# Optimization experiments

Measured on AMD Instinct MI355X. Metric: run time of the kernel, lower is better.

## Reference

```python
import jax, jax.numpy as jnp
import numpy as np

B = 16384
C = 1000  # num_classes
H = 128   # adapter hidden


def setup_inputs() -> dict:
    key = jax.random.key(0)
    k1, k2, k3 = jax.random.split(key, 3)
    logits = jax.random.normal(k1, (B, C), dtype=jnp.float32)
    # adapter_net params: Linear(C->H) -> ReLU -> Linear(H->C); stored as x @ W + b
    W1 = jax.random.normal(k2, (C, H), dtype=jnp.float32) * 0.03
    b1 = jnp.zeros((H,), dtype=jnp.float32)
    W2 = jax.random.normal(k3, (H, C), dtype=jnp.float32) * 0.03
    b2 = jnp.zeros((C,), dtype=jnp.float32)
    return {"logits": logits, "W1": W1, "b1": b1, "W2": W2, "b2": b2}


def reference(logits, W1, b1, W2, b2):
    prob = jax.nn.softmax(logits, axis=-1)                       # [B, C]
    # descending sort
    order = jnp.argsort(-prob, axis=-1)                          # [B, C] int
    sorted_prob = jnp.take_along_axis(prob, order, axis=-1)      # [B, C]
    # diffs between consecutive sorted probs, last column = 1
    diffs = jnp.concatenate(
        [sorted_prob[:, :-1] - sorted_prob[:, 1:],
         jnp.ones((prob.shape[0], 1), dtype=prob.dtype)], axis=-1)
    # adapter net on prob
    h = jax.nn.relu(prob @ W1 + b1)                              # [B, H]
    cal = h @ W2 + b2                                            # [B, C]
    cal = jnp.concatenate([jax.nn.sigmoid(cal[:, :-1]), cal[:, -1:]], axis=-1)
    c = diffs * cal                                              # [B, C]
    # U @ c  (U upper-triangular ones) == reverse cumulative sum along last dim
    rev_cumsum = jnp.cumsum(c[:, ::-1], axis=-1)[:, ::-1]        # [B, C]
    # S.T @ v scatters sorted-position values back to original class positions
    inv_order = jnp.argsort(order, axis=-1)                      # inverse permutation
    fitted = jnp.take_along_axis(rev_cumsum, inv_order, axis=-1)
    return fitted + logits
```

## Files before the change

kernel.cpp:

```cpp
#include <hip/hip_runtime.h>
#include <hip/hip_bf16.h>
#include <math.h>

#define B_ROWS 16384
#define C_CLS  1000
#define H_DIM  128
#define NEG_BIG (-3.0e38f)

#define MT    16
#define PSTR  1064
#define CSTR  1064
#define HSTR  136
#define KT1   32
#define CT1   8
#define KT2   4
#define CT2   64

#define QSCALE 511.0f
#define QINV   (1.0f / 511.0f)

typedef __attribute__((ext_vector_type(8))) short short8;
typedef __attribute__((ext_vector_type(4))) float f32x4;

__device__ __forceinline__ unsigned short f2bf(float x) {
    unsigned int u = __float_as_uint(x);
    unsigned int r = (u + 0x7FFFu + ((u >> 16) & 1u)) >> 16;
    return (unsigned short)r;
}
__device__ __forceinline__ float bf2f(unsigned short v) {
    return __uint_as_float(((unsigned int)v) << 16);
}
__device__ __forceinline__ float sigm(float x) {
    return 1.0f / (1.0f + __expf(-x));
}
__device__ __forceinline__ unsigned int umin(unsigned int a, unsigned int b) {
    return a < b ? a : b;
}
__device__ __forceinline__ int SKU(int i) { return i + (i >> 4); }
__device__ __forceinline__ int PSL(unsigned int b) {
    return (int)((b >> 3) + (b & 7u) * 64u);
}

__global__ __launch_bounds__(256) void pack_kernel(
    const float* __restrict__ W1, const float* __restrict__ W2,
    unsigned short* __restrict__ W1p, unsigned short* __restrict__ W2p)
{
    const int t = blockIdx.x * 256 + threadIdx.x;
    if (t < 16384) {
        const int lane = t & 63, slot = t >> 6;
        const int kt = slot >> 3, ct = slot & 7;
        const int col = ct * 16 + (lane & 15);
        const int k0 = kt * 32 + (lane >> 4) * 8;
        unsigned short v[8];
        #pragma unroll
        for (int j = 0; j < 8; ++j) {
            int k = k0 + j;
            v[j] = f2bf((k < C_CLS) ? W1[k * H_DIM + col] : 0.f);
        }
        #pragma unroll
        for (int j = 0; j < 8; ++j) W1p[(size_t)t * 8 + j] = v[j];
    } else {
        const int t2 = t - 16384;
        const int lane = t2 & 63, slot = t2 >> 6;
        const int kt = slot >> 6, ct = slot & 63;
        const int col = ct * 16 + (lane & 15);
        const int k0 = kt * 32 + (lane >> 4) * 8;
        unsigned short v[8];
        #pragma unroll
        for (int j = 0; j < 8; ++j) {
            int k = k0 + j;
            v[j] = f2bf((col < C_CLS) ? W2[k * C_CLS + col] : 0.f);
        }
        #pragma unroll
        for (int j = 0; j < 8; ++j) W2p[(size_t)t2 * 8 + j] = v[j];
    }
}

__global__ __launch_bounds__(512) void fused_kernel(
    const float* __restrict__ logits, const float* __restrict__ bias1,
    const float* __restrict__ bias2, const unsigned short* __restrict__ W1p,
    const unsigned short* __restrict__ W2p, float* __restrict__ out)
{
    __shared__ alignas(16) unsigned short probS[MT * PSTR];
    __shared__ alignas(16) unsigned int uniReg[8 * 512];
    __shared__ float qsA[MT], svsA[MT], rowInv[MT], rowLast[MT];

    unsigned short* calS = probS;
    unsigned short* hS = (unsigned short*)uniReg;

    const int tid = threadIdx.x;
    const int w = tid >> 6, lane = tid & 63;
    const size_t row0 = (size_t)blockIdx.x * MT;

    #pragma unroll
    for (int rr = 0; rr < 2; ++rr) {
        const int r = 2 * w + rr;
        const float* lr = logits + (row0 + r) * C_CLS;
        float sum = 0.f, mx = NEG_BIG;
        for (int c4 = lane; c4 < 250; c4 += 64) {
            const float4 x = reinterpret_cast<const float4*>(lr)[c4];
            float e0 = __expf(x.x), e1 = __expf(x.y);
            float e2 = __expf(x.z), e3 = __expf(x.w);
            sum += (e0 + e1) + (e2 + e3);
            mx = fmaxf(mx, fmaxf(fmaxf(x.x, x.y), fmaxf(x.z, x.w)));
            uint2 pk;
            asm("v_cvt_pk_bf16_f32 %0, %1, %2" : "=v"(pk.x) : "v"(e0), "v"(e1));
            asm("v_cvt_pk_bf16_f32 %0, %1, %2" : "=v"(pk.y) : "v"(e2), "v"(e3));
            *reinterpret_cast<uint2*>(&probS[r * PSTR + 4 * c4]) = pk;
        }
        #pragma unroll
        for (int off = 32; off; off >>= 1) {
            sum += __shfl_xor(sum, off);
            mx = fmaxf(mx, __shfl_xor(mx, off));
        }
        if (lane == 0) {
            const float maxe = __expf(mx);
            rowInv[r] = 1.0f / sum;
            qsA[r]  = QSCALE / maxe;
            svsA[r] = maxe * QINV * (1.0f / sum);
        }
        if (lane < 12) *reinterpret_cast<unsigned int*>(&probS[r * PSTR + 1000 + 2 * lane]) = 0u;
    }
    __syncthreads();

    {
        f32x4 acc = {0.f, 0.f, 0.f, 0.f};
        const unsigned short* aptr = probS + (lane & 15) * PSTR + (lane >> 4) * 8;
        #pragma unroll 4
        for (int kt = 0; kt < KT1; ++kt) {
            short8 a = *reinterpret_cast<const short8*>(aptr + kt * 32);
            short8 b = *reinterpret_cast<const short8*>(W1p + ((size_t)(kt * CT1 + w) * 64 + lane) * 8);
            acc = __builtin_amdgcn_mfma_f32_16x16x32_bf16(a, b, acc, 0, 0, 0);
        }
        const int hc = w * 16 + (lane & 15);
        const float bb = bias1[hc];
        #pragma unroll
        for (int i = 0; i < 4; ++i) {
            const int hrow = (lane >> 4) * 4 + i;
            hS[hrow * HSTR + hc] = f2bf(fmaxf(acc[i] * rowInv[hrow] + bb, 0.f));
        }
    }

    unsigned int dP[2][8];
    #pragma unroll
    for (int rr = 0; rr < 2; ++rr) {
        const int r = 2 * w + rr;
        const float qs = qsA[r];
        #pragma unroll
        for (int k = 0; k < 8; ++k) {
            const unsigned int pk =
                *reinterpret_cast<const unsigned int*>(&probS[r * PSTR + 2 * lane + 128 * k]);
            unsigned int d0 = umin((unsigned int)(bf2f((unsigned short)(pk & 0xFFFFu)) * qs), 511u);
            unsigned int d1 = umin((unsigned int)(bf2f((unsigned short)(pk >> 16)) * qs), 511u);
            dP[rr][k] = d0 | (d1 << 16);
        }
    }
    __syncthreads();

    {
        f32x4 acc[8];
        #pragma unroll
        for (int t = 0; t < 8; ++t) acc[t] = (f32x4){0.f, 0.f, 0.f, 0.f};
        const unsigned short* haptr = hS + (lane & 15) * HSTR + (lane >> 4) * 8;
        #pragma unroll
        for (int kt = 0; kt < KT2; ++kt) {
            short8 a = *reinterpret_cast<const short8*>(haptr + kt * 32);
            #pragma unroll
            for (int t = 0; t < 8; ++t) {
                short8 b = *reinterpret_cast<const short8*>(
                    W2p + ((size_t)(kt * CT2 + 8 * w + t) * 64 + lane) * 8);
                acc[t] = __builtin_amdgcn_mfma_f32_16x16x32_bf16(a, b, acc[t], 0, 0, 0);
            }
        }
        #pragma unroll
        for (int t = 0; t < 8; ++t) {
            const int col = (8 * w + t) * 16 + (lane & 15);
            if (col < C_CLS) {
                const int sc = SKU(col);
                #pragma unroll
                for (int i = 0; i < 4; ++i) {
                    const int rloc = (lane >> 4) * 4 + i;
                    float v = acc[t][i] + bias2[col];
                    calS[rloc * CSTR + sc] = f2bf(v);
                    if (col == C_CLS - 1) rowLast[rloc] = v;
                }
            }
        }
    }
    __syncthreads();

    unsigned int* hist = uniReg + w * 512;
    float* Pb = (float*)(uniReg + w * 512);
    const bool act7 = lane < 52;

    #pragma unroll
    for (int rr = 0; rr < 2; ++rr) {
        const int r = 2 * w + rr;
        const float svs = svsA[r];
        const size_t rowbase = (row0 + r) * C_CLS;

        #pragma unroll
        for (int k = 0; k < 4; ++k) hist[64 * k + lane] = 0u;

        #pragma unroll
        for (int k = 0; k < 8; ++k) {
            if (k < 7 || act7) {
                const unsigned int d0 = dP[rr][k] & 0xFFFFu;
                const unsigned int d1 = dP[rr][k] >> 16;
                atomicAdd(&hist[d0 >> 1], 1u << ((d0 & 1u) * 16u));
                atomicAdd(&hist[d1 >> 1], 1u << ((d1 & 1u) * 16u));
            }
        }

        unsigned int c[8], T;
        unsigned int base0;
        {
            uint4 v = *reinterpret_cast<uint4*>(&hist[4 * lane]);
            c[0] = v.x & 0xFFFFu; c[1] = v.x >> 16;
            c[2] = v.y & 0xFFFFu; c[3] = v.y >> 16;
            c[4] = v.z & 0xFFFFu; c[5] = v.z >> 16;
            c[6] = v.w & 0xFFFFu; c[7] = v.w >> 16;
            T = ((c[0] + c[1]) + (c[2] + c[3])) + ((c[4] + c[5]) + (c[6] + c[7]));
            unsigned int x = T;
            #pragma unroll
            for (int off = 1; off < 64; off <<= 1) {
                unsigned int y = __shfl_up(x, off);
                if (lane >= off) x += y;
            }
            base0 = x - T;
        }

        int prev;
        {
            int hiOcc = -1;
            #pragma unroll
            for (int j = 0; j < 8; ++j) if (c[j] > 0) hiOcc = 8 * lane + j;
            int x = hiOcc;
            #pragma unroll
            for (int off = 1; off < 64; off <<= 1) {
                int y = __shfl_up(x, off);
                if (lane >= off) x = max(x, y);
            }
            prev = __shfl_up(x, 1);
            if (lane == 0) prev = -1;
        }

        float s[8];
        float run = 0.f;
        {
            unsigned int brun = base0;
            #pragma unroll
            for (int j = 0; j < 8; ++j) {
                const int b = 8 * lane + j;
                float e = 0.f;
                if (c[j] > 0) {
                    if (brun == 0) {
                        e = rowLast[r];
                    } else {
                        const float cl = bf2f(calS[r * CSTR + SKU((C_CLS - 1) - (int)brun)]);
                        e = (float)(b - prev) * svs * sigm(cl);
                    }
                    prev = b;
                }
                brun += c[j];
                run += e;
                s[j] = run;
            }
        }
        float x = run;
        #pragma unroll
        for (int off = 1; off < 64; off <<= 1) {
            float y = __shfl_up(x, off);
            if (lane >= off) x += y;
        }
        const float X = x - run;

        #pragma unroll
        for (int j = 0; j < 8; ++j) Pb[lane + 64 * j] = X + s[j];

        #pragma unroll
        for (int k = 0; k < 8; ++k) {
            if (k < 7 || act7) {
                const int idx = 2 * lane + 128 * k;
                const float2 xf = *reinterpret_cast<const float2*>(&logits[rowbase + idx]);
                float2 ov;
                ov.x = Pb[PSL(dP[rr][k] & 0xFFFFu)] + xf.x;
                ov.y = Pb[PSL(dP[rr][k] >> 16)] + xf.y;
                *reinterpret_cast<float2*>(&out[rowbase + idx]) = ov;
            }
        }
    }
}

extern "C" void kernel_launch(void* const* d_in, const int* in_sizes, int n_in,
                              void* d_out, int out_size, void* d_ws, size_t ws_size,
                              hipStream_t stream)
{
    const float* logits = (const float*)d_in[0];
    const float* W1     = (const float*)d_in[1];
    const float* b1     = (const float*)d_in[2];
    const float* W2     = (const float*)d_in[3];
    const float* b2     = (const float*)d_in[4];
    float* out = (float*)d_out;

    unsigned short* W1p = (unsigned short*)d_ws;
    unsigned short* W2p = W1p + (size_t)KT1 * CT1 * 64 * 8;

    pack_kernel<<<dim3(128), dim3(256), 0, stream>>>(W1, W2, W1p, W2p);

    fused_kernel<<<dim3(B_ROWS / MT), dim3(512), 0, stream>>>(
        logits, b1, b2, W1p, W2p, out);
}
```

Baseline: 68.14 us.

## Interleave two rows per wave in rank/scatter phase and prefetch logits early

Each wave now processes its two rows at the same time through histogram, scans and scatter, keeping separate shared-memory histogram buffers per row. This gives the scan shuffles more independent work to overlap. The second-pass logits loads are issued at the start of the phase so their global latency hides behind the histogram work. The Pb stride is padded from 64 to 68 to cut LDS bank conflicts. The cost is more registers (32 float2 prefetches plus doubled state) and more shared memory, which may lower occupancy.

```diff
diff --git a/kernel.cpp b/kernel.cpp
--- a/kernel.cpp
+++ b/kernel.cpp
@@ -15,6 +15,7 @@
 #define CT1   8
 #define KT2   4
 #define CT2   64
+#define SLICE 576
 
 #define QSCALE 511.0f
 #define QINV   (1.0f / 511.0f)
@@ -38,7 +39,7 @@
 }
 __device__ __forceinline__ int SKU(int i) { return i + (i >> 4); }
 __device__ __forceinline__ int PSL(unsigned int b) {
-    return (int)((b >> 3) + (b & 7u) * 64u);
+    return (int)((b >> 3) + (b & 7u) * 68u);
 }
 
 __global__ __launch_bounds__(256) void pack_kernel(
@@ -82,7 +83,7 @@
     const unsigned short* __restrict__ W2p, float* __restrict__ out)
 {
     __shared__ alignas(16) unsigned short probS[MT * PSTR];
-    __shared__ alignas(16) unsigned int uniReg[8 * 512];
+    __shared__ alignas(16) unsigned int uniReg[8 * 2 * SLICE];
     __shared__ float qsA[MT], svsA[MT], rowInv[MT], rowLast[MT];
 
     unsigned short* calS = probS;
@@ -189,105 +190,137 @@
     }
     __syncthreads();
 
-    unsigned int* hist = uniReg + w * 512;
-    float* Pb = (float*)(uniReg + w * 512);
+    unsigned int* hist0 = uniReg + (size_t)w * 2 * SLICE;
+    unsigned int* hist1 = hist0 + SLICE;
+    float* Pb0 = (float*)hist0;
+    float* Pb1 = (float*)hist1;
     const bool act7 = lane < 52;
-
+    const size_t rowbase0 = (row0 + 2 * w) * C_CLS;
+    const size_t rowbase1 = rowbase0 + C_CLS;
+
+    float2 xf[2][8];
+    #pragma unroll
+    for (int k = 0; k < 8; ++k) {
+        if (k < 7 || act7) {
+            xf[0][k] = *reinterpret_cast<const float2*>(&logits[rowbase0 + 2 * lane + 128 * k]);
+            xf[1][k] = *reinterpret_cast<const float2*>(&logits[rowbase1 + 2 * lane + 128 * k]);
+        }
+    }
+
+    #pragma unroll
+    for (int k = 0; k < 4; ++k) {
+        hist0[64 * k + lane] = 0u;
+        hist1[64 * k + lane] = 0u;
+    }
+
+    #pragma unroll
+    for (int k = 0; k < 8; ++k) {
+        if (k < 7 || act7) {
+            const unsigned int a0 = dP[0][k] & 0xFFFFu, a1 = dP[0][k] >> 16;
+            atomicAdd(&hist0[a0 >> 1], 1u << ((a0 & 1u) * 16u));
+            atomicAdd(&hist0[a1 >> 1], 1u << ((a1 & 1u) * 16u));
+            const unsigned int b0 = dP[1][k] & 0xFFFFu, b1 = dP[1][k] >> 16;
+            atomicAdd(&hist1[b0 >> 1], 1u << ((b0 & 1u) * 16u));
+            atomicAdd(&hist1[b1 >> 1], 1u << ((b1 & 1u) * 16u));
+        }
+    }
+
+    unsigned int c[2][8], T[2];
+    #pragma unroll
+    for (int rr = 0; rr < 2; ++rr) {
+        uint4 v = *reinterpret_cast<uint4*>(&(rr ? hist1 : hist0)[4 * lane]);
+        c[rr][0] = v.x & 0xFFFFu; c[rr][1] = v.x >> 16;
+        c[rr][2] = v.y & 0xFFFFu; c[rr][3] = v.y >> 16;
+        c[rr][4] = v.z & 0xFFFFu; c[rr][5] = v.z >> 16;
+        c[rr][6] = v.w & 0xFFFFu; c[rr][7] = v.w >> 16;
+        T[rr] = ((c[rr][0] + c[rr][1]) + (c[rr][2] + c[rr][3]))
+              + ((c[rr][4] + c[rr][5]) + (c[rr][6] + c[rr][7]));
+    }
+
+    unsigned int base0_[2];
+    int prev_[2];
+    {
+        unsigned int x0 = T[0], x1 = T[1];
+        int h0 = -1, h1 = -1;
+        #pragma unroll
+        for (int j = 0; j < 8; ++j) {
+            if (c[0][j] > 0) h0 = 8 * lane + j;
+            if (c[1][j] > 0) h1 = 8 * lane + j;
+        }
+        int m0 = h0, m1 = h1;
+        #pragma unroll
+        for (int off = 1; off < 64; off <<= 1) {
+            unsigned int y0 = __shfl_up(x0, off);
+            unsigned int y1 = __shfl_up(x1, off);
+            int n0 = __shfl_up(m0, off);
+            int n1 = __shfl_up(m1, off);
+            if (lane >= off) { x0 += y0; x1 += y1; m0 = max(m0, n0); m1 = max(m1, n1); }
+        }
+        base0_[0] = x0 - T[0];
+        base0_[1] = x1 - T[1];
+        prev_[0] = __shfl_up(m0, 1);
+        prev_[1] = __shfl_up(m1, 1);
+        if (lane == 0) { prev_[0] = -1; prev_[1] = -1; }
+    }
+
+    float s[2][8], run_[2];
     #pragma unroll
     for (int rr = 0; rr < 2; ++rr) {
         const int r = 2 * w + rr;
         const float svs = svsA[r];
-        const size_t rowbase = (row0 + r) * C_CLS;
-
-        #pragma unroll
-        for (int k = 0; k < 4; ++k) hist[64 * k + lane] = 0u;
-
-        #pragma unroll
-        for (int k = 0; k < 8; ++k) {
-            if (k < 7 || act7) {
-                const unsigned int d0 = dP[rr][k] & 0xFFFFu;
-                const unsigned int d1 = dP[rr][k] >> 16;
-                atomicAdd(&hist[d0 >> 1], 1u << ((d0 & 1u) * 16u));
-                atomicAdd(&hist[d1 >> 1], 1u << ((d1 & 1u) * 16u));
+        unsigned int brun = base0_[rr];
+        int prev = prev_[rr];
+        float run = 0.f;
+        #pragma unroll
+        for (int j = 0; j < 8; ++j) {
+            const int b = 8 * lane + j;
+            float e = 0.f;
+            if (c[rr][j] > 0) {
+                if (brun == 0) {
+                    e = rowLast[r];
+                } else {
+                    const float cl = bf2f(calS[r * CSTR + SKU((C_CLS - 1) - (int)brun)]);
+                    e = (float)(b - prev) * svs * sigm(cl);
+                }
+                prev = b;
             }
-        }
-
-        unsigned int c[8], T;
-        unsigned int base0;
-        {
-            uint4 v = *reinterpret_cast<uint4*>(&hist[4 * lane]);
-            c[0] = v.x & 0xFFFFu; c[1] = v.x >> 16;
-            c[2] = v.y & 0xFFFFu; c[3] = v.y >> 16;
-            c[4] = v.z & 0xFFFFu; c[5] = v.z >> 16;
-            c[6] = v.w & 0xFFFFu; c[7] = v.w >> 16;
-            T = ((c[0] + c[1]) + (c[2] + c[3])) + ((c[4] + c[5]) + (c[6] + c[7]));
-            unsigned int x = T;
-            #pragma unroll
-            for (int off = 1; off < 64; off <<= 1) {
-                unsigned int y = __shfl_up(x, off);
-                if (lane >= off) x += y;
-            }
-            base0 = x - T;
-        }
-
-        int prev;
-        {
-            int hiOcc = -1;
-            #pragma unroll
-            for (int j = 0; j < 8; ++j) if (c[j] > 0) hiOcc = 8 * lane + j;
-            int x = hiOcc;
-            #pragma unroll
-            for (int off = 1; off < 64; off <<= 1) {
-                int y = __shfl_up(x, off);
-                if (lane >= off) x = max(x, y);
-            }
-            prev = __shfl_up(x, 1);
-            if (lane == 0) prev = -1;
-        }
-
-        float s[8];
-        float run = 0.f;
-        {
-            unsigned int brun = base0;
-            #pragma unroll
-            for (int j = 0; j < 8; ++j) {
-                const int b = 8 * lane + j;
-                float e = 0.f;
-                if (c[j] > 0) {
-                    if (brun == 0) {
-                        e = rowLast[r];
-                    } else {
-                        const float cl = bf2f(calS[r * CSTR + SKU((C_CLS - 1) - (int)brun)]);
-                        e = (float)(b - prev) * svs * sigm(cl);
-                    }
-                    prev = b;
-                }
-                brun += c[j];
-                run += e;
-                s[j] = run;
-            }
-        }
-        float x = run;
+            brun += c[rr][j];
+            run += e;
+            s[rr][j] = run;
+        }
+        run_[rr] = run;
+    }
+
+    float X_[2];
+    {
+        float x0 = run_[0], x1 = run_[1];
         #pragma unroll
         for (int off = 1; off < 64; off <<= 1) {
-            float y = __shfl_up(x, off);
-            if (lane >= off) x += y;
-        }
-        const float X = x - run;
-
-        #pragma unroll
-        for (int j = 0; j < 8; ++j) Pb[lane + 64 * j] = X + s[j];
-
-        #pragma unroll
-        for (int k = 0; k < 8; ++k) {
-            if (k < 7 || act7) {
-                const int idx = 2 * lane + 128 * k;
-                const float2 xf = *reinterpret_cast<const float2*>(&logits[rowbase + idx]);
-                float2 ov;
-                ov.x = Pb[PSL(dP[rr][k] & 0xFFFFu)] + xf.x;
-                ov.y = Pb[PSL(dP[rr][k] >> 16)] + xf.y;
-                *reinterpret_cast<float2*>(&out[rowbase + idx]) = ov;
-            }
+            float y0 = __shfl_up(x0, off);
+            float y1 = __shfl_up(x1, off);
+            if (lane >= off) { x0 += y0; x1 += y1; }
+        }
+        X_[0] = x0 - run_[0];
+        X_[1] = x1 - run_[1];
+    }
+
+    #pragma unroll
+    for (int j = 0; j < 8; ++j) {
+        Pb0[lane + 68 * j] = X_[0] + s[0][j];
+        Pb1[lane + 68 * j] = X_[1] + s[1][j];
+    }
+
+    #pragma unroll
+    for (int k = 0; k < 8; ++k) {
+        if (k < 7 || act7) {
+            const int idx = 2 * lane + 128 * k;
+            float2 ov0, ov1;
+            ov0.x = Pb0[PSL(dP[0][k] & 0xFFFFu)] + xf[0][k].x;
+            ov0.y = Pb0[PSL(dP[0][k] >> 16)] + xf[0][k].y;
+            ov1.x = Pb1[PSL(dP[1][k] & 0xFFFFu)] + xf[1][k].x;
+            ov1.y = Pb1[PSL(dP[1][k] >> 16)] + xf[1][k].y;
+            *reinterpret_cast<float2*>(&out[rowbase0 + idx]) = ov0;
+            *reinterpret_cast<float2*>(&out[rowbase1 + idx]) = ov1;
         }
     }
 }
```

Result: faster. 65.11 us (-4.4%).

## Use one wavefront per row with 1024-thread blocks and padded per-row scratch

Applied to the files above, without the earlier changes.

Doubles block size to 16 wavefronts so each wavefront owns a single row instead of two, splitting the second GEMM's column tiles across all 16 waves. Only the first 8 waves run the first GEMM. Each row gets its own padded LDS slice, with PSL stride changed from 64 to 68 to reduce bank conflicts. Logits for the output phase are prefetched into registers before the histogram work, so the global load latency overlaps with it. The aim is more parallelism per block and shorter serial per-row work. The costs are a larger LDS footprint, idle waves during GEMM1, and register pressure from the 1024-thread launch bound.

```diff
diff --git a/kernel.cpp b/kernel.cpp
--- a/kernel.cpp
+++ b/kernel.cpp
@@ -15,6 +15,7 @@
 #define CT1   8
 #define KT2   4
 #define CT2   64
+#define SLICE 576
 
 #define QSCALE 511.0f
 #define QINV   (1.0f / 511.0f)
@@ -38,7 +39,7 @@
 }
 __device__ __forceinline__ int SKU(int i) { return i + (i >> 4); }
 __device__ __forceinline__ int PSL(unsigned int b) {
-    return (int)((b >> 3) + (b & 7u) * 64u);
+    return (int)((b >> 3) + (b & 7u) * 68u);
 }
 
 __global__ __launch_bounds__(256) void pack_kernel(
@@ -76,13 +77,13 @@
     }
 }
 
-__global__ __launch_bounds__(512) void fused_kernel(
+__global__ __launch_bounds__(1024, 8) void fused_kernel(
     const float* __restrict__ logits, const float* __restrict__ bias1,
     const float* __restrict__ bias2, const unsigned short* __restrict__ W1p,
     const unsigned short* __restrict__ W2p, float* __restrict__ out)
 {
     __shared__ alignas(16) unsigned short probS[MT * PSTR];
-    __shared__ alignas(16) unsigned int uniReg[8 * 512];
+    __shared__ alignas(16) unsigned int uniReg[MT * SLICE];
     __shared__ float qsA[MT], svsA[MT], rowInv[MT], rowLast[MT];
 
     unsigned short* calS = probS;
@@ -91,10 +92,9 @@
     const int tid = threadIdx.x;
     const int w = tid >> 6, lane = tid & 63;
     const size_t row0 = (size_t)blockIdx.x * MT;
-
-    #pragma unroll
-    for (int rr = 0; rr < 2; ++rr) {
-        const int r = 2 * w + rr;
+    const int r = w;
+
+    {
         const float* lr = logits + (row0 + r) * C_CLS;
         float sum = 0.f, mx = NEG_BIG;
         for (int c4 = lane; c4 < 250; c4 += 64) {
@@ -123,7 +123,7 @@
     }
     __syncthreads();
 
-    {
+    if (w < 8) {
         f32x4 acc = {0.f, 0.f, 0.f, 0.f};
         const unsigned short* aptr = probS + (lane & 15) * PSTR + (lane >> 4) * 8;
         #pragma unroll 4
@@ -141,10 +141,8 @@
         }
     }
 
-    unsigned int dP[2][8];
-    #pragma unroll
-    for (int rr = 0; rr < 2; ++rr) {
-        const int r = 2 * w + rr;
+    unsigned int dP[8];
+    {
         const float qs = qsA[r];
         #pragma unroll
         for (int k = 0; k < 8; ++k) {
@@ -152,29 +150,29 @@
                 *reinterpret_cast<const unsigned int*>(&probS[r * PSTR + 2 * lane + 128 * k]);
             unsigned int d0 = umin((unsigned int)(bf2f((unsigned short)(pk & 0xFFFFu)) * qs), 511u);
             unsigned int d1 = umin((unsigned int)(bf2f((unsigned short)(pk >> 16)) * qs), 511u);
-            dP[rr][k] = d0 | (d1 << 16);
+            dP[k] = d0 | (d1 << 16);
         }
     }
     __syncthreads();
 
     {
-        f32x4 acc[8];
-        #pragma unroll
-        for (int t = 0; t < 8; ++t) acc[t] = (f32x4){0.f, 0.f, 0.f, 0.f};
+        f32x4 acc[4];
+        #pragma unroll
+        for (int t = 0; t < 4; ++t) acc[t] = (f32x4){0.f, 0.f, 0.f, 0.f};
         const unsigned short* haptr = hS + (lane & 15) * HSTR + (lane >> 4) * 8;
         #pragma unroll
         for (int kt = 0; kt < KT2; ++kt) {
             short8 a = *reinterpret_cast<const short8*>(haptr + kt * 32);
             #pragma unroll
-            for (int t = 0; t < 8; ++t) {
+            for (int t = 0; t < 4; ++t) {
                 short8 b = *reinterpret_cast<const short8*>(
-                    W2p + ((size_t)(kt * CT2 + 8 * w + t) * 64 + lane) * 8);
+                    W2p + ((size_t)(kt * CT2 + 4 * w + t) * 64 + lane) * 8);
                 acc[t] = __builtin_amdgcn_mfma_f32_16x16x32_bf16(a, b, acc[t], 0, 0, 0);
             }
         }
         #pragma unroll
-        for (int t = 0; t < 8; ++t) {
-            const int col = (8 * w + t) * 16 + (lane & 15);
+        for (int t = 0; t < 4; ++t) {
+            const int col = (4 * w + t) * 16 + (lane & 15);
             if (col < C_CLS) {
                 const int sc = SKU(col);
                 #pragma unroll
@@ -189,105 +187,100 @@
     }
     __syncthreads();
 
-    unsigned int* hist = uniReg + w * 512;
-    float* Pb = (float*)(uniReg + w * 512);
+    unsigned int* hist = uniReg + (size_t)w * SLICE;
+    float* Pb = (float*)hist;
     const bool act7 = lane < 52;
-
-    #pragma unroll
-    for (int rr = 0; rr < 2; ++rr) {
-        const int r = 2 * w + rr;
-        const float svs = svsA[r];
-        const size_t rowbase = (row0 + r) * C_CLS;
-
-        #pragma unroll
-        for (int k = 0; k < 4; ++k) hist[64 * k + lane] = 0u;
-
-        #pragma unroll
-        for (int k = 0; k < 8; ++k) {
-            if (k < 7 || act7) {
-                const unsigned int d0 = dP[rr][k] & 0xFFFFu;
-                const unsigned int d1 = dP[rr][k] >> 16;
-                atomicAdd(&hist[d0 >> 1], 1u << ((d0 & 1u) * 16u));
-                atomicAdd(&hist[d1 >> 1], 1u << ((d1 & 1u) * 16u));
+    const size_t rowbase = (row0 + r) * C_CLS;
+    const float svs = svsA[r];
+
+    float2 xf[8];
+    #pragma unroll
+    for (int k = 0; k < 8; ++k) {
+        if (k < 7 || act7) {
+            xf[k] = *reinterpret_cast<const float2*>(&logits[rowbase + 2 * lane + 128 * k]);
+        }
+    }
+
+    #pragma unroll
+    for (int k = 0; k < 4; ++k) hist[64 * k + lane] = 0u;
+
+    #pragma unroll
+    for (int k = 0; k < 8; ++k) {
+        if (k < 7 || act7) {
+            const unsigned int d0 = dP[k] & 0xFFFFu;
+            const unsigned int d1 = dP[k] >> 16;
+            atomicAdd(&hist[d0 >> 1], 1u << ((d0 & 1u) * 16u));
+            atomicAdd(&hist[d1 >> 1], 1u << ((d1 & 1u) * 16u));
+        }
+    }
+
+    unsigned int c[8], T;
+    unsigned int base0;
+    int prev;
+    {
+        uint4 v = *reinterpret_cast<uint4*>(&hist[4 * lane]);
+        c[0] = v.x & 0xFFFFu; c[1] = v.x >> 16;
+        c[2] = v.y & 0xFFFFu; c[3] = v.y >> 16;
+        c[4] = v.z & 0xFFFFu; c[5] = v.z >> 16;
+        c[6] = v.w & 0xFFFFu; c[7] = v.w >> 16;
+        T = ((c[0] + c[1]) + (c[2] + c[3])) + ((c[4] + c[5]) + (c[6] + c[7]));
+        int hiOcc = -1;
+        #pragma unroll
+        for (int j = 0; j < 8; ++j) if (c[j] > 0) hiOcc = 8 * lane + j;
+        unsigned int x = T;
+        int m = hiOcc;
+        #pragma unroll
+        for (int off = 1; off < 64; off <<= 1) {
+            unsigned int y = __shfl_up(x, off);
+            int n = __shfl_up(m, off);
+            if (lane >= off) { x += y; m = max(m, n); }
+        }
+        base0 = x - T;
+        prev = __shfl_up(m, 1);
+        if (lane == 0) prev = -1;
+    }
+
+    float s[8];
+    float run = 0.f;
+    {
+        unsigned int brun = base0;
+        #pragma unroll
+        for (int j = 0; j < 8; ++j) {
+            const int b = 8 * lane + j;
+            float e = 0.f;
+            if (c[j] > 0) {
+                if (brun == 0) {
+                    e = rowLast[r];
+                } else {
+                    const float cl = bf2f(calS[r * CSTR + SKU((C_CLS - 1) - (int)brun)]);
+                    e = (float)(b - prev) * svs * sigm(cl);
+                }
+                prev = b;
             }
-        }
-
-        unsigned int c[8], T;
-        unsigned int base0;
-        {
-            uint4 v = *reinterpret_cast<uint4*>(&hist[4 * lane]);
-            c[0] = v.x & 0xFFFFu; c[1] = v.x >> 16;
-            c[2] = v.y & 0xFFFFu; c[3] = v.y >> 16;
-            c[4] = v.z & 0xFFFFu; c[5] = v.z >> 16;
-            c[6] = v.w & 0xFFFFu; c[7] = v.w >> 16;
-            T = ((c[0] + c[1]) + (c[2] + c[3])) + ((c[4] + c[5]) + (c[6] + c[7]));
-            unsigned int x = T;
-            #pragma unroll
-            for (int off = 1; off < 64; off <<= 1) {
-                unsigned int y = __shfl_up(x, off);
-                if (lane >= off) x += y;
-            }
-            base0 = x - T;
-        }
-
-        int prev;
-        {
-            int hiOcc = -1;
-            #pragma unroll
-            for (int j = 0; j < 8; ++j) if (c[j] > 0) hiOcc = 8 * lane + j;
-            int x = hiOcc;
-            #pragma unroll
-            for (int off = 1; off < 64; off <<= 1) {
-                int y = __shfl_up(x, off);
-                if (lane >= off) x = max(x, y);
-            }
-            prev = __shfl_up(x, 1);
-            if (lane == 0) prev = -1;
-        }
-
-        float s[8];
-        float run = 0.f;
-        {
-            unsigned int brun = base0;
-            #pragma unroll
-            for (int j = 0; j < 8; ++j) {
-                const int b = 8 * lane + j;
-                float e = 0.f;
-                if (c[j] > 0) {
-                    if (brun == 0) {
-                        e = rowLast[r];
-                    } else {
-                        const float cl = bf2f(calS[r * CSTR + SKU((C_CLS - 1) - (int)brun)]);
-                        e = (float)(b - prev) * svs * sigm(cl);
-                    }
-                    prev = b;
-                }
-                brun += c[j];
-                run += e;
-                s[j] = run;
-            }
-        }
-        float x = run;
-        #pragma unroll
-        for (int off = 1; off < 64; off <<= 1) {
-            float y = __shfl_up(x, off);
-            if (lane >= off) x += y;
-        }
-        const float X = x - run;
-
-        #pragma unroll
-        for (int j = 0; j < 8; ++j) Pb[lane + 64 * j] = X + s[j];
-
-        #pragma unroll
-        for (int k = 0; k < 8; ++k) {
-            if (k < 7 || act7) {
-                const int idx = 2 * lane + 128 * k;
-                const float2 xf = *reinterpret_cast<const float2*>(&logits[rowbase + idx]);
-                float2 ov;
-                ov.x = Pb[PSL(dP[rr][k] & 0xFFFFu)] + xf.x;
-                ov.y = Pb[PSL(dP[rr][k] >> 16)] + xf.y;
-                *reinterpret_cast<float2*>(&out[rowbase + idx]) = ov;
-            }
+            brun += c[j];
+            run += e;
+            s[j] = run;
+        }
+    }
+    float x = run;
+    #pragma unroll
+    for (int off = 1; off < 64; off <<= 1) {
+        float y = __shfl_up(x, off);
+        if (lane >= off) x += y;
+    }
+    const float X = x - run;
+
+    #pragma unroll
+    for (int j = 0; j < 8; ++j) Pb[lane + 68 * j] = X + s[j];
+
+    #pragma unroll
+    for (int k = 0; k < 8; ++k) {
+        if (k < 7 || act7) {
+            const int idx = 2 * lane + 128 * k;
+            float2 ov;
+            ov.x = Pb[PSL(dP[k] & 0xFFFFu)] + xf[k].x;
+            ov.y = Pb[PSL(dP[k] >> 16)] + xf[k].y;
+            *reinterpret_cast<float2*>(&out[rowbase + idx]) = ov;
         }
     }
 }
@@ -308,6 +301,6 @@
 
     pack_kernel<<<dim3(128), dim3(256), 0, stream>>>(W1, W2, W1p, W2p);
 
-    fused_kernel<<<dim3(B_ROWS / MT), dim3(512), 0, stream>>>(
+    fused_kernel<<<dim3(B_ROWS / MT), dim3(1024), 0, stream>>>(
         logits, b1, b2, W1p, W2p, out);
 }
```

Result: slower. 70.51 us (+3.5%).
